# Performance work log

Hardware: AMD Instinct MI355X
Metric: run time of the kernel (lower is better)

Reference implementation:

```python
import jax, jax.numpy as jnp
import numpy as np

N = 100000
K = 27  # 3^3 kernel offsets for dimension=3
EPS = 1e-6


def layer_norm(x, gamma, beta):
    mu = jnp.mean(x, axis=-1, keepdims=True)
    var = jnp.mean(jnp.square(x - mu), axis=-1, keepdims=True)
    return (x - mu) * jax.lax.rsqrt(var + EPS) * gamma + beta


def sparse_conv3(x, idx, mask, W):
    # gather-GEMM-scatter form of Minkowski sparse conv:
    # x: [N, Cin], idx/mask: [N, K], W: [K, Cin, Cout]
    xg = jnp.where(mask[..., None], x[idx], 0.0)  # [N, K, Cin]
    return jnp.einsum('nkc,kcd->nd', xg, W)


def setup_inputs() -> dict:
    key = jax.random.key(0)
    ks = jax.random.split(key, 6)
    x = jax.random.normal(ks[0], (N, 32), dtype=jnp.float32)
    neighbor_idx = jax.random.randint(ks[1], (N, K), 0, N, dtype=jnp.int32)
    neighbor_mask = jax.random.randint(ks[2], (N, K), 0, 2) > 0
    W_conv = jax.random.normal(ks[3], (32, 32), dtype=jnp.float32) * 0.1
    W1 = jax.random.normal(ks[4], (K, 32, 128), dtype=jnp.float32) * 0.05
    W2 = jax.random.normal(ks[5], (K, 128, 32), dtype=jnp.float32) * 0.05
    return {
        'x': x,
        'neighbor_idx': neighbor_idx,
        'neighbor_mask': neighbor_mask,
        'W_conv': W_conv,
        'gamma0': jnp.ones((32,), jnp.float32),
        'beta0': jnp.zeros((32,), jnp.float32),
        'W1': W1,
        'gamma1': jnp.ones((128,), jnp.float32),
        'beta1': jnp.zeros((128,), jnp.float32),
        'W2': W2,
        'gamma2': jnp.ones((32,), jnp.float32),
        'beta2': jnp.zeros((32,), jnp.float32),
    }


def reference(x, neighbor_idx, neighbor_mask, W_conv, gamma0, beta0,
              W1, gamma1, beta1, W2, gamma2, beta2):
    gelu = lambda t: jax.nn.gelu(t, approximate=False)  # torch default (erf)
    residual = x
    out = x @ W_conv                      # kernel_size=1 conv == dense matmul
    out = gelu(layer_norm(out, gamma0, beta0))
    out = sparse_conv3(out, neighbor_idx, neighbor_mask, W1)
    out = gelu(layer_norm(out, gamma1, beta1))
    out = sparse_conv3(out, neighbor_idx, neighbor_mask, W2)
    out = layer_norm(out, gamma2, beta2)
    out = out + residual
    return gelu(out)
```

## Files before the change

### kernel.cpp

```cpp
#include <hip/hip_runtime.h>
#include <hip/hip_bf16.h>
#include <math.h>

#define NPTS 100000
#define KOFF 27

typedef __attribute__((ext_vector_type(8))) __bf16 bf16x8;
typedef __attribute__((ext_vector_type(4))) float f32x4;

__device__ __forceinline__ unsigned short f2bf(float f) {
    unsigned int u = __float_as_uint(f);
    u += 0x7fffu + ((u >> 16) & 1u);
    return (unsigned short)(u >> 16);
}

__device__ __forceinline__ float gelu_erf(float v) {
    return 0.5f * v * (1.0f + erff(v * 0.70710678118654752f));
}

__global__ __launch_bounds__(256)
void repack_kernel(const float* __restrict__ W1, const float* __restrict__ W2,
                   const void* __restrict__ maskp,
                   unsigned short* __restrict__ W1p,
                   unsigned short* __restrict__ W2p,
                   int* __restrict__ flagp) {
    int o = blockIdx.x * 256 + threadIdx.x;
    if (o == 0) {
        const unsigned int* mw = (const unsigned int*)maskp;
        int f = 0;
        for (int i = 0; i < 64; ++i) f |= (mw[i] > 1u) ? 1 : 0;
        *flagp = f;
    }
    if (o < KOFF * 32 * 128) {
        int j = o & 7, lane = (o >> 3) & 63;
        int quad = lane >> 4, nn = lane & 15;
        int ct1 = (o >> 9) & 7, k1 = o >> 12;
        int kk1 = quad * 8 + j;
        W1p[o] = f2bf(W1[(k1 * 32 + kk1) * 128 + (ct1 * 16 + nn)]);
        int ct2 = (o >> 9) & 1, kc2 = (o >> 10) & 3, k2 = o >> 12;
        int kk2 = kc2 * 32 + quad * 8 + j;
        W2p[o] = f2bf(W2[(k2 * 128 + kk2) * 32 + (ct2 * 16 + nn)]);
    }
}

__global__ __launch_bounds__(256)
void conv1_ln_gelu(const float* __restrict__ x, const float* __restrict__ Wc,
                   const float* __restrict__ g0, const float* __restrict__ b0,
                   unsigned short* __restrict__ out0) {
    __shared__ float xs[256];
    __shared__ float wc[1024];
    int t = threadIdx.x;
    int nb = blockIdx.x * 8;
    xs[t] = x[nb * 32 + t];
    for (int i = t; i < 1024; i += 256) wc[i] = Wc[i];
    __syncthreads();
    int r = t >> 5, d = t & 31;
    const float* xr = &xs[r * 32];
    float v = 0.f;
#pragma unroll
    for (int c = 0; c < 32; ++c) v = fmaf(xr[c], wc[c * 32 + d], v);
    float s = v, s2 = v * v;
#pragma unroll
    for (int m = 16; m >= 1; m >>= 1) {
        s  += __shfl_xor(s,  m, 32);
        s2 += __shfl_xor(s2, m, 32);
    }
    float mu  = s * (1.f / 32.f);
    float var = s2 * (1.f / 32.f) - mu * mu;
    float y = (v - mu) * rsqrtf(var + 1e-6f) * g0[d] + b0[d];
    out0[nb * 32 + t] = f2bf(gelu_erf(y));
}

__device__ __forceinline__ void stage_gidx(int* s_gidx, const int* nidx,
                                           const void* maskp, int mflag,
                                           int nb, int t) {
    int cnt = (NPTS - nb < 64 ? NPTS - nb : 64) * KOFF;
    for (int i = t; i < 64 * KOFF; i += 256) {
        int g = -1;
        if (i < cnt) {
            int gi = nidx[nb * KOFF + i];
            int m = mflag ? (int)((const unsigned char*)maskp)[nb * KOFF + i]
                          : ((const int*)maskp)[nb * KOFF + i];
            g = m ? gi : -1;
        }
        s_gidx[i] = g;
    }
}

__global__ __launch_bounds__(256, 4)
void conv_k1(const int* __restrict__ nidx, const void* __restrict__ maskp,
             const int* __restrict__ flagp,
             const unsigned short* __restrict__ out0,
             const unsigned short* __restrict__ W1p,
             const float* __restrict__ g1, const float* __restrict__ b1,
             unsigned short* __restrict__ out1) {
    __shared__ int   s_gidx[64 * KOFF];
    __shared__ float s_g[128], s_b[128];

    int t = threadIdx.x;
    int nb = blockIdx.x * 64;
    int mflag = *flagp;
    if (t < 128) { s_g[t] = g1[t]; s_b[t] = b1[t]; }
    stage_gidx(s_gidx, nidx, maskp, mflag, nb, t);
    __syncthreads();

    int lane = t & 63, w = t >> 6;
    int mrow = lane & 15, quad = lane >> 4;
    const int* gp = &s_gidx[(w * 16 + mrow) * KOFF];

    f32x4 acc[8] = {};
    int gnxt = gp[1];
    {
        int g0i = gp[0];
        bf16x8 tmp = {};
        if (g0i >= 0) tmp = *reinterpret_cast<const bf16x8*>(out0 + g0i * 32 + quad * 8);
        bf16x8 a_nxt = tmp;
        for (int k = 0; k < KOFF; ++k) {
            bf16x8 a_cur = a_nxt;
            int gtmp = gnxt;
            gnxt = gp[k + 2 < KOFF ? k + 2 : KOFF - 1];
            a_nxt = bf16x8{};
            if (gtmp >= 0)
                a_nxt = *reinterpret_cast<const bf16x8*>(out0 + gtmp * 32 + quad * 8);
            const unsigned short* wb = W1p + (((k * 8) * 64 + lane) << 3);
#pragma unroll
            for (int ct = 0; ct < 8; ++ct) {
                bf16x8 bfr = *reinterpret_cast<const bf16x8*>(wb + ((ct * 64) << 3));
                acc[ct] = __builtin_amdgcn_mfma_f32_16x16x32_bf16(a_cur, bfr, acc[ct], 0, 0, 0);
            }
        }
    }

    int n_base = nb + w * 16 + quad * 4;
#pragma unroll
    for (int r = 0; r < 4; ++r) {
        float s = 0.f, s2 = 0.f;
#pragma unroll
        for (int ct = 0; ct < 8; ++ct) { float v = acc[ct][r]; s += v; s2 += v * v; }
#pragma unroll
        for (int m = 1; m <= 8; m <<= 1) {
            s  += __shfl_xor(s,  m, 16);
            s2 += __shfl_xor(s2, m, 16);
        }
        float mu = s * (1.f / 128.f);
        float rs = rsqrtf(s2 * (1.f / 128.f) - mu * mu + 1e-6f);
        int n = n_base + r;
        if (n < NPTS) {
#pragma unroll
            for (int ct = 0; ct < 8; ++ct) {
                int c = ct * 16 + mrow;
                float y = (acc[ct][r] - mu) * rs * s_g[c] + s_b[c];
                out1[n * 128 + c] = f2bf(gelu_erf(y));
            }
        }
    }
}

__global__ __launch_bounds__(256, 4)
void conv_k2(const int* __restrict__ nidx, const void* __restrict__ maskp,
             const int* __restrict__ flagp,
             const unsigned short* __restrict__ out1,
             const unsigned short* __restrict__ W2p,
             const float* __restrict__ g2, const float* __restrict__ b2,
             const float* __restrict__ x, float* __restrict__ outp) {
    __shared__ int   s_gidx[64 * KOFF];
    __shared__ float s_g[32], s_b[32];

    int t = threadIdx.x;
    int nb = blockIdx.x * 64;
    int mflag = *flagp;
    if (t < 32) { s_g[t] = g2[t]; s_b[t] = b2[t]; }
    stage_gidx(s_gidx, nidx, maskp, mflag, nb, t);
    __syncthreads();

    int lane = t & 63, w = t >> 6;
    int mrow = lane & 15, quad = lane >> 4;
    const int* gp = &s_gidx[(w * 16 + mrow) * KOFF];

    f32x4 acc[2] = {};
    int gnxt = gp[1];
    bf16x8 a_nxt[4] = {};
    {
        int g0i = gp[0];
        if (g0i >= 0) {
#pragma unroll
            for (int kc = 0; kc < 4; ++kc)
                a_nxt[kc] = *reinterpret_cast<const bf16x8*>(out1 + g0i * 128 + kc * 32 + quad * 8);
        }
    }
    for (int k = 0; k < KOFF; ++k) {
        bf16x8 a_cur[4];
#pragma unroll
        for (int kc = 0; kc < 4; ++kc) a_cur[kc] = a_nxt[kc];
        int gtmp = gnxt;
        gnxt = gp[k + 2 < KOFF ? k + 2 : KOFF - 1];
#pragma unroll
        for (int kc = 0; kc < 4; ++kc) a_nxt[kc] = bf16x8{};
        if (gtmp >= 0) {
#pragma unroll
            for (int kc = 0; kc < 4; ++kc)
                a_nxt[kc] = *reinterpret_cast<const bf16x8*>(out1 + gtmp * 128 + kc * 32 + quad * 8);
        }
        const unsigned short* wb = W2p + (((k * 8) * 64 + lane) << 3);
#pragma unroll
        for (int kc = 0; kc < 4; ++kc) {
            bf16x8 b0 = *reinterpret_cast<const bf16x8*>(wb + (((kc * 2 + 0) * 64) << 3));
            bf16x8 b1 = *reinterpret_cast<const bf16x8*>(wb + (((kc * 2 + 1) * 64) << 3));
            acc[0] = __builtin_amdgcn_mfma_f32_16x16x32_bf16(a_cur[kc], b0, acc[0], 0, 0, 0);
            acc[1] = __builtin_amdgcn_mfma_f32_16x16x32_bf16(a_cur[kc], b1, acc[1], 0, 0, 0);
        }
    }

    int n_base = nb + w * 16 + quad * 4;
#pragma unroll
    for (int r = 0; r < 4; ++r) {
        float v0 = acc[0][r], v1 = acc[1][r];
        float s = v0 + v1, s2 = v0 * v0 + v1 * v1;
#pragma unroll
        for (int m = 1; m <= 8; m <<= 1) {
            s  += __shfl_xor(s,  m, 16);
            s2 += __shfl_xor(s2, m, 16);
        }
        float mu = s * (1.f / 32.f);
        float rs = rsqrtf(s2 * (1.f / 32.f) - mu * mu + 1e-6f);
        int n = n_base + r;
        if (n < NPTS) {
            int c0 = mrow, c1 = mrow + 16;
            float y0 = (v0 - mu) * rs * s_g[c0] + s_b[c0] + x[n * 32 + c0];
            float y1 = (v1 - mu) * rs * s_g[c1] + s_b[c1] + x[n * 32 + c1];
            outp[n * 32 + c0] = gelu_erf(y0);
            outp[n * 32 + c1] = gelu_erf(y1);
        }
    }
}

extern "C" void kernel_launch(void* const* d_in, const int* in_sizes, int n_in,
                              void* d_out, int out_size, void* d_ws, size_t ws_size,
                              hipStream_t stream) {
    const float* x    = (const float*)d_in[0];
    const int*   nidx = (const int*)d_in[1];
    const void*  maskp = d_in[2];
    const float* Wc = (const float*)d_in[3];
    const float* g0 = (const float*)d_in[4];
    const float* b0 = (const float*)d_in[5];
    const float* W1 = (const float*)d_in[6];
    const float* g1 = (const float*)d_in[7];
    const float* b1 = (const float*)d_in[8];
    const float* W2 = (const float*)d_in[9];
    const float* g2 = (const float*)d_in[10];
    const float* b2 = (const float*)d_in[11];

    char* ws = (char*)d_ws;
    unsigned short* out0 = (unsigned short*)ws;
    unsigned short* out1 = (unsigned short*)(ws + 6400000);
    unsigned short* W1p  = (unsigned short*)(ws + 32000000);
    unsigned short* W2p  = W1p + KOFF * 32 * 128;
    int* flagp = (int*)(W2p + KOFF * 128 * 32);

    repack_kernel<<<432, 256, 0, stream>>>(W1, W2, maskp, W1p, W2p, flagp);
    conv1_ln_gelu<<<NPTS / 8, 256, 0, stream>>>(x, Wc, g0, b0, out0);
    conv_k1<<<(NPTS + 63) / 64, 256, 0, stream>>>(nidx, maskp, flagp, out0, W1p, g1, b1, out1);
    conv_k2<<<(NPTS + 63) / 64, 256, 0, stream>>>(nidx, maskp, flagp, out1, W2p, g2, b2, x, (float*)d_out);
}
```

Baseline: 289.7 us.

## Use zero sentinel row for masked neighbors and deepen gather prefetch

Masked neighbors now point to an extra zeroed row at index NPTS in the out0/out1 buffers, set up by the repack kernel. This removes the per-offset branch and conditional zeroing from the gather loops. The gather pipeline is deepened to 6 offsets ahead in conv_k1 and 4 ahead in conv_k2, with the K loop fully unrolled. More loads stay in flight to hide random-gather latency, at the cost of more registers, which may cut occupancy in conv_k2.

Measured after the change: 314.2 us. +8.5%, slower.

```diff
diff --git a/kernel.cpp b/kernel.cpp
--- a/kernel.cpp
+++ b/kernel.cpp
@@ -23,13 +23,20 @@
                    const void* __restrict__ maskp,
                    unsigned short* __restrict__ W1p,
                    unsigned short* __restrict__ W2p,
-                   int* __restrict__ flagp) {
+                   int* __restrict__ flagp,
+                   unsigned short* __restrict__ out0,
+                   unsigned short* __restrict__ out1) {
     int o = blockIdx.x * 256 + threadIdx.x;
-    if (o == 0) {
-        const unsigned int* mw = (const unsigned int*)maskp;
-        int f = 0;
-        for (int i = 0; i < 64; ++i) f |= (mw[i] > 1u) ? 1 : 0;
-        *flagp = f;
+    if (blockIdx.x == 0) {
+        int t = threadIdx.x;
+        if (t == 0) {
+            const unsigned int* mw = (const unsigned int*)maskp;
+            int f = 0;
+            for (int i = 0; i < 64; ++i) f |= (mw[i] > 1u) ? 1 : 0;
+            *flagp = f;
+        }
+        if (t < 32)  out0[NPTS * 32 + t] = 0;
+        if (t < 128) out1[NPTS * 128 + t] = 0;
     }
     if (o < KOFF * 32 * 128) {
         int j = o & 7, lane = (o >> 3) & 63;
@@ -76,12 +83,12 @@
                                            int nb, int t) {
     int cnt = (NPTS - nb < 64 ? NPTS - nb : 64) * KOFF;
     for (int i = t; i < 64 * KOFF; i += 256) {
-        int g = -1;
+        int g = NPTS;
         if (i < cnt) {
             int gi = nidx[nb * KOFF + i];
             int m = mflag ? (int)((const unsigned char*)maskp)[nb * KOFF + i]
                           : ((const int*)maskp)[nb * KOFF + i];
-            g = m ? gi : -1;
+            g = m ? gi : NPTS;
         }
         s_gidx[i] = g;
     }
@@ -107,28 +114,24 @@
     int lane = t & 63, w = t >> 6;
     int mrow = lane & 15, quad = lane >> 4;
     const int* gp = &s_gidx[(w * 16 + mrow) * KOFF];
+    const unsigned short* a_base = out0 + quad * 8;
 
     f32x4 acc[8] = {};
-    int gnxt = gp[1];
-    {
-        int g0i = gp[0];
-        bf16x8 tmp = {};
-        if (g0i >= 0) tmp = *reinterpret_cast<const bf16x8*>(out0 + g0i * 32 + quad * 8);
-        bf16x8 a_nxt = tmp;
-        for (int k = 0; k < KOFF; ++k) {
-            bf16x8 a_cur = a_nxt;
-            int gtmp = gnxt;
-            gnxt = gp[k + 2 < KOFF ? k + 2 : KOFF - 1];
-            a_nxt = bf16x8{};
-            if (gtmp >= 0)
-                a_nxt = *reinterpret_cast<const bf16x8*>(out0 + gtmp * 32 + quad * 8);
-            const unsigned short* wb = W1p + (((k * 8) * 64 + lane) << 3);
-#pragma unroll
-            for (int ct = 0; ct < 8; ++ct) {
-                bf16x8 bfr = *reinterpret_cast<const bf16x8*>(wb + ((ct * 64) << 3));
-                acc[ct] = __builtin_amdgcn_mfma_f32_16x16x32_bf16(a_cur, bfr, acc[ct], 0, 0, 0);
-            }
-        }
+    bf16x8 a_pf[6];
+#pragma unroll
+    for (int d = 0; d < 6; ++d)
+        a_pf[d] = *reinterpret_cast<const bf16x8*>(a_base + gp[d] * 32);
+
+#pragma unroll
+    for (int k = 0; k < KOFF; ++k) {
+        const unsigned short* wb = W1p + (((k * 8) * 64 + lane) << 3);
+#pragma unroll
+        for (int ct = 0; ct < 8; ++ct) {
+            bf16x8 bfr = *reinterpret_cast<const bf16x8*>(wb + ((ct * 64) << 3));
+            acc[ct] = __builtin_amdgcn_mfma_f32_16x16x32_bf16(a_pf[k % 6], bfr, acc[ct], 0, 0, 0);
+        }
+        int kn = (k + 6 < KOFF) ? k + 6 : KOFF - 1;
+        a_pf[k % 6] = *reinterpret_cast<const bf16x8*>(a_base + gp[kn] * 32);
     }
 
     int n_base = nb + w * 16 + quad * 4;
@@ -176,39 +179,33 @@
     int lane = t & 63, w = t >> 6;
     int mrow = lane & 15, quad = lane >> 4;
     const int* gp = &s_gidx[(w * 16 + mrow) * KOFF];
+    const unsigned short* a_base = out1 + quad * 8;
 
     f32x4 acc[2] = {};
-    int gnxt = gp[1];
-    bf16x8 a_nxt[4] = {};
-    {
-        int g0i = gp[0];
-        if (g0i >= 0) {
-#pragma unroll
-            for (int kc = 0; kc < 4; ++kc)
-                a_nxt[kc] = *reinterpret_cast<const bf16x8*>(out1 + g0i * 128 + kc * 32 + quad * 8);
-        }
-    }
+    bf16x8 a_pf[4][4];
+#pragma unroll
+    for (int d = 0; d < 4; ++d) {
+        int g = gp[d];
+#pragma unroll
+        for (int kc = 0; kc < 4; ++kc)
+            a_pf[d][kc] = *reinterpret_cast<const bf16x8*>(a_base + g * 128 + kc * 32);
+    }
+
+#pragma unroll
     for (int k = 0; k < KOFF; ++k) {
-        bf16x8 a_cur[4];
-#pragma unroll
-        for (int kc = 0; kc < 4; ++kc) a_cur[kc] = a_nxt[kc];
-        int gtmp = gnxt;
-        gnxt = gp[k + 2 < KOFF ? k + 2 : KOFF - 1];
-#pragma unroll
-        for (int kc = 0; kc < 4; ++kc) a_nxt[kc] = bf16x8{};
-        if (gtmp >= 0) {
-#pragma unroll
-            for (int kc = 0; kc < 4; ++kc)
-                a_nxt[kc] = *reinterpret_cast<const bf16x8*>(out1 + gtmp * 128 + kc * 32 + quad * 8);
-        }
         const unsigned short* wb = W2p + (((k * 8) * 64 + lane) << 3);
 #pragma unroll
         for (int kc = 0; kc < 4; ++kc) {
             bf16x8 b0 = *reinterpret_cast<const bf16x8*>(wb + (((kc * 2 + 0) * 64) << 3));
             bf16x8 b1 = *reinterpret_cast<const bf16x8*>(wb + (((kc * 2 + 1) * 64) << 3));
-            acc[0] = __builtin_amdgcn_mfma_f32_16x16x32_bf16(a_cur[kc], b0, acc[0], 0, 0, 0);
-            acc[1] = __builtin_amdgcn_mfma_f32_16x16x32_bf16(a_cur[kc], b1, acc[1], 0, 0, 0);
-        }
+            acc[0] = __builtin_amdgcn_mfma_f32_16x16x32_bf16(a_pf[k % 4][kc], b0, acc[0], 0, 0, 0);
+            acc[1] = __builtin_amdgcn_mfma_f32_16x16x32_bf16(a_pf[k % 4][kc], b1, acc[1], 0, 0, 0);
+        }
+        int kn = (k + 4 < KOFF) ? k + 4 : KOFF - 1;
+        int g = gp[kn];
+#pragma unroll
+        for (int kc = 0; kc < 4; ++kc)
+            a_pf[k % 4][kc] = *reinterpret_cast<const bf16x8*>(a_base + g * 128 + kc * 32);
     }
 
     int n_base = nb + w * 16 + quad * 4;
@@ -252,12 +249,12 @@
 
     char* ws = (char*)d_ws;
     unsigned short* out0 = (unsigned short*)ws;
-    unsigned short* out1 = (unsigned short*)(ws + 6400000);
-    unsigned short* W1p  = (unsigned short*)(ws + 32000000);
+    unsigned short* out1 = (unsigned short*)(ws + 6400128);
+    unsigned short* W1p  = (unsigned short*)(ws + 32000512);
     unsigned short* W2p  = W1p + KOFF * 32 * 128;
     int* flagp = (int*)(W2p + KOFF * 128 * 32);
 
-    repack_kernel<<<432, 256, 0, stream>>>(W1, W2, maskp, W1p, W2p, flagp);
+    repack_kernel<<<432, 256, 0, stream>>>(W1, W2, maskp, W1p, W2p, flagp, out0, out1);
     conv1_ln_gelu<<<NPTS / 8, 256, 0, stream>>>(x, Wc, g0, b0, out0);
     conv_k1<<<(NPTS + 63) / 64, 256, 0, stream>>>(nidx, maskp, flagp, out0, W1p, g1, b1, out1);
     conv_k2<<<(NPTS + 63) / 64, 256, 0, stream>>>(nidx, maskp, flagp, out1, W2p, g2, b2, x, (float*)d_out);
```

## Use one wave per 64-row block with register-double-buffered gathers and weights

Applied to the files above, without the earlier changes.

Both sparse conv kernels change from four waves of 16 rows each to a single 64-thread wave that computes all 64 rows as four 16-row MFMA tiles. Each weight fragment is then loaded once per wave and reused across four row tiles, cutting redundant weight loads. Gathered activations and weights for the next offset are loaded into registers while the current offset's MFMAs run, and the offset loop is fully unrolled. The cost is much higher register pressure (acc[4][8] in conv_k1, large a/b double buffers in conv_k2) and far fewer waves per CU, so there is less latency hiding for the random gathers.

Result: faster. 276.9 us (-4.4%).

```diff
diff --git a/kernel.cpp b/kernel.cpp
--- a/kernel.cpp
+++ b/kernel.cpp
@@ -71,11 +71,11 @@
     out0[nb * 32 + t] = f2bf(gelu_erf(y));
 }
 
-__device__ __forceinline__ void stage_gidx(int* s_gidx, const int* nidx,
-                                           const void* maskp, int mflag,
-                                           int nb, int t) {
+__device__ __forceinline__ void stage_gidx64(int* s_gidx, const int* nidx,
+                                             const void* maskp, int mflag,
+                                             int nb, int t) {
     int cnt = (NPTS - nb < 64 ? NPTS - nb : 64) * KOFF;
-    for (int i = t; i < 64 * KOFF; i += 256) {
+    for (int i = t; i < 64 * KOFF; i += 64) {
         int g = -1;
         if (i < cnt) {
             int gi = nidx[nb * KOFF + i];
@@ -87,149 +87,194 @@
     }
 }
 
-__global__ __launch_bounds__(256, 4)
+__global__ __launch_bounds__(64, 2)
 void conv_k1(const int* __restrict__ nidx, const void* __restrict__ maskp,
              const int* __restrict__ flagp,
              const unsigned short* __restrict__ out0,
              const unsigned short* __restrict__ W1p,
              const float* __restrict__ g1, const float* __restrict__ b1,
              unsigned short* __restrict__ out1) {
-    __shared__ int   s_gidx[64 * KOFF];
-    __shared__ float s_g[128], s_b[128];
+    __shared__ int s_gidx[64 * KOFF];
 
     int t = threadIdx.x;
     int nb = blockIdx.x * 64;
     int mflag = *flagp;
-    if (t < 128) { s_g[t] = g1[t]; s_b[t] = b1[t]; }
-    stage_gidx(s_gidx, nidx, maskp, mflag, nb, t);
+    stage_gidx64(s_gidx, nidx, maskp, mflag, nb, t);
     __syncthreads();
 
-    int lane = t & 63, w = t >> 6;
+    int lane = t & 63;
     int mrow = lane & 15, quad = lane >> 4;
-    const int* gp = &s_gidx[(w * 16 + mrow) * KOFF];
-
-    f32x4 acc[8] = {};
-    int gnxt = gp[1];
+    const unsigned short* a_base = out0 + quad * 8;
+    const int* gp0 = &s_gidx[(0 * 16 + mrow) * KOFF];
+    const int* gp1 = &s_gidx[(1 * 16 + mrow) * KOFF];
+    const int* gp2 = &s_gidx[(2 * 16 + mrow) * KOFF];
+    const int* gp3 = &s_gidx[(3 * 16 + mrow) * KOFF];
+
+    f32x4 acc[4][8] = {};
+    bf16x8 a[2][4], b[2][8];
+
     {
-        int g0i = gp[0];
-        bf16x8 tmp = {};
-        if (g0i >= 0) tmp = *reinterpret_cast<const bf16x8*>(out0 + g0i * 32 + quad * 8);
-        bf16x8 a_nxt = tmp;
-        for (int k = 0; k < KOFF; ++k) {
-            bf16x8 a_cur = a_nxt;
-            int gtmp = gnxt;
-            gnxt = gp[k + 2 < KOFF ? k + 2 : KOFF - 1];
-            a_nxt = bf16x8{};
-            if (gtmp >= 0)
-                a_nxt = *reinterpret_cast<const bf16x8*>(out0 + gtmp * 32 + quad * 8);
-            const unsigned short* wb = W1p + (((k * 8) * 64 + lane) << 3);
-#pragma unroll
-            for (int ct = 0; ct < 8; ++ct) {
-                bf16x8 bfr = *reinterpret_cast<const bf16x8*>(wb + ((ct * 64) << 3));
-                acc[ct] = __builtin_amdgcn_mfma_f32_16x16x32_bf16(a_cur, bfr, acc[ct], 0, 0, 0);
-            }
-        }
-    }
-
-    int n_base = nb + w * 16 + quad * 4;
-#pragma unroll
-    for (int r = 0; r < 4; ++r) {
-        float s = 0.f, s2 = 0.f;
-#pragma unroll
-        for (int ct = 0; ct < 8; ++ct) { float v = acc[ct][r]; s += v; s2 += v * v; }
-#pragma unroll
-        for (int m = 1; m <= 8; m <<= 1) {
-            s  += __shfl_xor(s,  m, 16);
-            s2 += __shfl_xor(s2, m, 16);
-        }
-        float mu = s * (1.f / 128.f);
-        float rs = rsqrtf(s2 * (1.f / 128.f) - mu * mu + 1e-6f);
-        int n = n_base + r;
-        if (n < NPTS) {
-#pragma unroll
-            for (int ct = 0; ct < 8; ++ct) {
-                int c = ct * 16 + mrow;
-                float y = (acc[ct][r] - mu) * rs * s_g[c] + s_b[c];
-                out1[n * 128 + c] = f2bf(gelu_erf(y));
-            }
-        }
-    }
-}
-
-__global__ __launch_bounds__(256, 4)
+        const unsigned short* wb = W1p + (lane << 3);
+#pragma unroll
+        for (int ct = 0; ct < 8; ++ct)
+            b[0][ct] = *reinterpret_cast<const bf16x8*>(wb + ((ct * 64) << 3));
+        int g0 = gp0[0], g1i = gp1[0], g2 = gp2[0], g3 = gp3[0];
+        a[0][0] = bf16x8{}; if (g0  >= 0) a[0][0] = *reinterpret_cast<const bf16x8*>(a_base + g0  * 32);
+        a[0][1] = bf16x8{}; if (g1i >= 0) a[0][1] = *reinterpret_cast<const bf16x8*>(a_base + g1i * 32);
+        a[0][2] = bf16x8{}; if (g2  >= 0) a[0][2] = *reinterpret_cast<const bf16x8*>(a_base + g2  * 32);
+        a[0][3] = bf16x8{}; if (g3  >= 0) a[0][3] = *reinterpret_cast<const bf16x8*>(a_base + g3  * 32);
+    }
+
+#pragma unroll
+    for (int k = 0; k < KOFF; ++k) {
+        int cur = k & 1, nxt = cur ^ 1;
+        if (k + 1 < KOFF) {
+            const unsigned short* wb = W1p + ((((k + 1) * 8) * 64 + lane) << 3);
+#pragma unroll
+            for (int ct = 0; ct < 8; ++ct)
+                b[nxt][ct] = *reinterpret_cast<const bf16x8*>(wb + ((ct * 64) << 3));
+            int g0 = gp0[k + 1], g1i = gp1[k + 1], g2 = gp2[k + 1], g3 = gp3[k + 1];
+            a[nxt][0] = bf16x8{}; if (g0  >= 0) a[nxt][0] = *reinterpret_cast<const bf16x8*>(a_base + g0  * 32);
+            a[nxt][1] = bf16x8{}; if (g1i >= 0) a[nxt][1] = *reinterpret_cast<const bf16x8*>(a_base + g1i * 32);
+            a[nxt][2] = bf16x8{}; if (g2  >= 0) a[nxt][2] = *reinterpret_cast<const bf16x8*>(a_base + g2  * 32);
+            a[nxt][3] = bf16x8{}; if (g3  >= 0) a[nxt][3] = *reinterpret_cast<const bf16x8*>(a_base + g3  * 32);
+        }
+#pragma unroll
+        for (int rt = 0; rt < 4; ++rt)
+#pragma unroll
+            for (int ct = 0; ct < 8; ++ct)
+                acc[rt][ct] = __builtin_amdgcn_mfma_f32_16x16x32_bf16(a[cur][rt], b[cur][ct], acc[rt][ct], 0, 0, 0);
+    }
+
+    float gv[8], bv[8];
+#pragma unroll
+    for (int ct = 0; ct < 8; ++ct) {
+        gv[ct] = g1[ct * 16 + mrow];
+        bv[ct] = b1[ct * 16 + mrow];
+    }
+#pragma unroll
+    for (int rt = 0; rt < 4; ++rt) {
+        int n_base = nb + rt * 16 + quad * 4;
+#pragma unroll
+        for (int r = 0; r < 4; ++r) {
+            float s = 0.f, s2 = 0.f;
+#pragma unroll
+            for (int ct = 0; ct < 8; ++ct) { float v = acc[rt][ct][r]; s += v; s2 += v * v; }
+#pragma unroll
+            for (int m = 1; m <= 8; m <<= 1) {
+                s  += __shfl_xor(s,  m, 16);
+                s2 += __shfl_xor(s2, m, 16);
+            }
+            float mu = s * (1.f / 128.f);
+            float rs = rsqrtf(s2 * (1.f / 128.f) - mu * mu + 1e-6f);
+            int n = n_base + r;
+            if (n < NPTS) {
+#pragma unroll
+                for (int ct = 0; ct < 8; ++ct) {
+                    float y = (acc[rt][ct][r] - mu) * rs * gv[ct] + bv[ct];
+                    out1[n * 128 + ct * 16 + mrow] = f2bf(gelu_erf(y));
+                }
+            }
+        }
+    }
+}
+
+__global__ __launch_bounds__(64, 2)
 void conv_k2(const int* __restrict__ nidx, const void* __restrict__ maskp,
              const int* __restrict__ flagp,
              const unsigned short* __restrict__ out1,
              const unsigned short* __restrict__ W2p,
              const float* __restrict__ g2, const float* __restrict__ b2,
              const float* __restrict__ x, float* __restrict__ outp) {
-    __shared__ int   s_gidx[64 * KOFF];
-    __shared__ float s_g[32], s_b[32];
+    __shared__ int s_gidx[64 * KOFF];
 
     int t = threadIdx.x;
     int nb = blockIdx.x * 64;
     int mflag = *flagp;
-    if (t < 32) { s_g[t] = g2[t]; s_b[t] = b2[t]; }
-    stage_gidx(s_gidx, nidx, maskp, mflag, nb, t);
+    stage_gidx64(s_gidx, nidx, maskp, mflag, nb, t);
     __syncthreads();
 
-    int lane = t & 63, w = t >> 6;
+    int lane = t & 63;
     int mrow = lane & 15, quad = lane >> 4;
-    const int* gp = &s_gidx[(w * 16 + mrow) * KOFF];
-
-    f32x4 acc[2] = {};
-    int gnxt = gp[1];
-    bf16x8 a_nxt[4] = {};
+    const unsigned short* a_base = out1 + quad * 8;
+    const int* gp0 = &s_gidx[(0 * 16 + mrow) * KOFF];
+    const int* gp1 = &s_gidx[(1 * 16 + mrow) * KOFF];
+    const int* gp2 = &s_gidx[(2 * 16 + mrow) * KOFF];
+    const int* gp3 = &s_gidx[(3 * 16 + mrow) * KOFF];
+
+    f32x4 acc[4][2] = {};
+    bf16x8 a[2][4][4], b[2][8];
+
     {
-        int g0i = gp[0];
-        if (g0i >= 0) {
-#pragma unroll
-            for (int kc = 0; kc < 4; ++kc)
-                a_nxt[kc] = *reinterpret_cast<const bf16x8*>(out1 + g0i * 128 + kc * 32 + quad * 8);
-        }
-    }
+        const unsigned short* wb = W2p + (lane << 3);
+#pragma unroll
+        for (int f = 0; f < 8; ++f)
+            b[0][f] = *reinterpret_cast<const bf16x8*>(wb + ((f * 64) << 3));
+        int gg[4] = { gp0[0], gp1[0], gp2[0], gp3[0] };
+#pragma unroll
+        for (int rt = 0; rt < 4; ++rt) {
+#pragma unroll
+            for (int kc = 0; kc < 4; ++kc) a[0][rt][kc] = bf16x8{};
+            if (gg[rt] >= 0) {
+#pragma unroll
+                for (int kc = 0; kc < 4; ++kc)
+                    a[0][rt][kc] = *reinterpret_cast<const bf16x8*>(a_base + gg[rt] * 128 + kc * 32);
+            }
+        }
+    }
+
+#pragma unroll
     for (int k = 0; k < KOFF; ++k) {
-        bf16x8 a_cur[4];
-#pragma unroll
-        for (int kc = 0; kc < 4; ++kc) a_cur[kc] = a_nxt[kc];
-        int gtmp = gnxt;
-        gnxt = gp[k + 2 < KOFF ? k + 2 : KOFF - 1];
-#pragma unroll
-        for (int kc = 0; kc < 4; ++kc) a_nxt[kc] = bf16x8{};
-        if (gtmp >= 0) {
-#pragma unroll
-            for (int kc = 0; kc < 4; ++kc)
-                a_nxt[kc] = *reinterpret_cast<const bf16x8*>(out1 + gtmp * 128 + kc * 32 + quad * 8);
-        }
-        const unsigned short* wb = W2p + (((k * 8) * 64 + lane) << 3);
-#pragma unroll
-        for (int kc = 0; kc < 4; ++kc) {
-            bf16x8 b0 = *reinterpret_cast<const bf16x8*>(wb + (((kc * 2 + 0) * 64) << 3));
-            bf16x8 b1 = *reinterpret_cast<const bf16x8*>(wb + (((kc * 2 + 1) * 64) << 3));
-            acc[0] = __builtin_amdgcn_mfma_f32_16x16x32_bf16(a_cur[kc], b0, acc[0], 0, 0, 0);
-            acc[1] = __builtin_amdgcn_mfma_f32_16x16x32_bf16(a_cur[kc], b1, acc[1], 0, 0, 0);
-        }
-    }
-
-    int n_base = nb + w * 16 + quad * 4;
-#pragma unroll
-    for (int r = 0; r < 4; ++r) {
-        float v0 = acc[0][r], v1 = acc[1][r];
-        float s = v0 + v1, s2 = v0 * v0 + v1 * v1;
-#pragma unroll
-        for (int m = 1; m <= 8; m <<= 1) {
-            s  += __shfl_xor(s,  m, 16);
-            s2 += __shfl_xor(s2, m, 16);
-        }
-        float mu = s * (1.f / 32.f);
-        float rs = rsqrtf(s2 * (1.f / 32.f) - mu * mu + 1e-6f);
-        int n = n_base + r;
-        if (n < NPTS) {
-            int c0 = mrow, c1 = mrow + 16;
-            float y0 = (v0 - mu) * rs * s_g[c0] + s_b[c0] + x[n * 32 + c0];
-            float y1 = (v1 - mu) * rs * s_g[c1] + s_b[c1] + x[n * 32 + c1];
-            outp[n * 32 + c0] = gelu_erf(y0);
-            outp[n * 32 + c1] = gelu_erf(y1);
+        int cur = k & 1, nxt = cur ^ 1;
+        if (k + 1 < KOFF) {
+            const unsigned short* wb = W2p + ((((k + 1) * 8) * 64 + lane) << 3);
+#pragma unroll
+            for (int f = 0; f < 8; ++f)
+                b[nxt][f] = *reinterpret_cast<const bf16x8*>(wb + ((f * 64) << 3));
+            int gg[4] = { gp0[k + 1], gp1[k + 1], gp2[k + 1], gp3[k + 1] };
+#pragma unroll
+            for (int rt = 0; rt < 4; ++rt) {
+#pragma unroll
+                for (int kc = 0; kc < 4; ++kc) a[nxt][rt][kc] = bf16x8{};
+                if (gg[rt] >= 0) {
+#pragma unroll
+                    for (int kc = 0; kc < 4; ++kc)
+                        a[nxt][rt][kc] = *reinterpret_cast<const bf16x8*>(a_base + gg[rt] * 128 + kc * 32);
+                }
+            }
+        }
+#pragma unroll
+        for (int rt = 0; rt < 4; ++rt)
+#pragma unroll
+            for (int kc = 0; kc < 4; ++kc) {
+                acc[rt][0] = __builtin_amdgcn_mfma_f32_16x16x32_bf16(a[cur][rt][kc], b[cur][kc * 2 + 0], acc[rt][0], 0, 0, 0);
+                acc[rt][1] = __builtin_amdgcn_mfma_f32_16x16x32_bf16(a[cur][rt][kc], b[cur][kc * 2 + 1], acc[rt][1], 0, 0, 0);
+            }
+    }
+
+    float gv0 = g2[mrow], gv1 = g2[mrow + 16];
+    float bv0 = b2[mrow], bv1 = b2[mrow + 16];
+#pragma unroll
+    for (int rt = 0; rt < 4; ++rt) {
+        int n_base = nb + rt * 16 + quad * 4;
+#pragma unroll
+        for (int r = 0; r < 4; ++r) {
+            float v0 = acc[rt][0][r], v1 = acc[rt][1][r];
+            float s = v0 + v1, s2 = v0 * v0 + v1 * v1;
+#pragma unroll
+            for (int m = 1; m <= 8; m <<= 1) {
+                s  += __shfl_xor(s,  m, 16);
+                s2 += __shfl_xor(s2, m, 16);
+            }
+            float mu = s * (1.f / 32.f);
+            float rs = rsqrtf(s2 * (1.f / 32.f) - mu * mu + 1e-6f);
+            int n = n_base + r;
+            if (n < NPTS) {
+                float y0 = (v0 - mu) * rs * gv0 + bv0 + x[n * 32 + mrow];
+                float y1 = (v1 - mu) * rs * gv1 + bv1 + x[n * 32 + mrow + 16];
+                outp[n * 32 + mrow]      = gelu_erf(y0);
+                outp[n * 32 + mrow + 16] = gelu_erf(y1);
+            }
         }
     }
 }
@@ -259,6 +304,6 @@
 
     repack_kernel<<<432, 256, 0, stream>>>(W1, W2, maskp, W1p, W2p, flagp);
     conv1_ln_gelu<<<NPTS / 8, 256, 0, stream>>>(x, Wc, g0, b0, out0);
-    conv_k1<<<(NPTS + 63) / 64, 256, 0, stream>>>(nidx, maskp, flagp, out0, W1p, g1, b1, out1);
-    conv_k2<<<(NPTS + 63) / 64, 256, 0, stream>>>(nidx, maskp, flagp, out1, W2p, g2, b2, x, (float*)d_out);
-}
+    conv_k1<<<(NPTS + 63) / 64, 64, 0, stream>>>(nidx, maskp, flagp, out0, W1p, g1, b1, out1);
+    conv_k2<<<(NPTS + 63) / 64, 64, 0, stream>>>(nidx, maskp, flagp, out1, W2p, g2, b2, x, (float*)d_out);
+}
```
